# Kernel tuning notes

Measured on AMD Instinct MI355X. Metric: run time of the kernel, lower is better.

Reference implementation:

```python
import jax, jax.numpy as jnp
import numpy as np

D_MODEL = 1024
N_HEADS = 16
HEAD_DIM = D_MODEL // N_HEADS


def setup_inputs() -> dict:
    key = jax.random.key(0)
    ks = jax.random.split(key, 5)
    B, S = 2, 2048
    x = jax.random.normal(ks[0], (B, S, D_MODEL), dtype=jnp.float32)
    # nn.Linear weights: [out_features, in_features]
    s_in = 1.0 / np.sqrt(D_MODEL)
    qkv_w = jax.random.uniform(ks[1], (3 * D_MODEL, D_MODEL), jnp.float32, -s_in, s_in)
    qkv_b = jax.random.uniform(ks[2], (3 * D_MODEL,), jnp.float32, -s_in, s_in)
    out_w = jax.random.uniform(ks[3], (D_MODEL, D_MODEL), jnp.float32, -s_in, s_in)
    out_b = jax.random.uniform(ks[4], (D_MODEL,), jnp.float32, -s_in, s_in)
    return {"x": x, "qkv_w": qkv_w, "qkv_b": qkv_b, "out_w": out_w, "out_b": out_b}


def reference(x, qkv_w, qkv_b, out_w, out_b):
    B, S, D = x.shape
    H, Hd = N_HEADS, HEAD_DIM
    scale = 1.0 / np.sqrt(Hd)
    qkv = jnp.einsum('bsd,ed->bse', x, qkv_w) + qkv_b  # [B,S,3D]
    qkv = qkv.reshape(B, S, 3, H, Hd)
    q = qkv[:, :, 0].transpose(0, 2, 1, 3)  # [B,H,S,Hd]
    k = qkv[:, :, 1].transpose(0, 2, 1, 3)
    v = qkv[:, :, 2].transpose(0, 2, 1, 3)
    scores = jnp.einsum('bhqd,bhkd->bhqk', q, k) * scale  # [B,H,S,S]
    causal = jnp.triu(jnp.ones((S, S), dtype=bool), k=1)
    scores = jnp.where(causal[None, None], -jnp.inf, scores)
    probs = jax.nn.softmax(scores, axis=-1)
    out = jnp.einsum('bhqk,bhkd->bhqd', probs, v)  # [B,H,S,Hd]
    out = out.transpose(0, 2, 1, 3).reshape(B, S, D)
    out = jnp.einsum('bsd,ed->bse', out, out_w) + out_b
    return out
```

## Files before the change

### kernel.cpp

```cpp
#include <hip/hip_runtime.h>
#include <hip/hip_bf16.h>

#define SEQ    2048
#define DMODEL 1024
#define NHEAD  16
#define HDIM   64
#define BATCH  2
#define NTOK   (BATCH * SEQ)

#define N_X   (NTOK * DMODEL)
#define N_WQ  (3 * DMODEL * DMODEL)
#define N_BQ  (3 * DMODEL)
#define N_WO  (DMODEL * DMODEL)
#define N_BO  (DMODEL)
#define N_CANON (N_X + N_WQ + N_BQ + N_WO + N_BO)

#define NEG_SENT (-1.0e30f)
#define QSCALE 0.1803368801111f

typedef __attribute__((ext_vector_type(8))) short short8;
typedef __attribute__((ext_vector_type(4))) short short4v;
typedef __attribute__((ext_vector_type(4))) float f32x4;

#define MFMA_BF16(A, B, C) __builtin_amdgcn_mfma_f32_16x16x32_bf16((A), (B), (C), 0, 0, 0)

static __device__ __forceinline__ short8 load8(const __hip_bfloat16* p) {
    return *(const short8*)p;
}

static __device__ __forceinline__ void async16(const void* g, void* l) {
    __builtin_amdgcn_global_load_lds(
        (const __attribute__((address_space(1))) unsigned int*)g,
        (__attribute__((address_space(3))) unsigned int*)l,
        16, 0, 0);
}

__global__ void detect_kernel(const unsigned short* __restrict__ w, int* flag) {
    int cnt = 0;
    for (int i = threadIdx.x; i < 512; i += 64) {
        const unsigned e = (w[i] >> 7) & 0xFF;
        if (e >= 125) cnt++;
    }
#pragma unroll
    for (int o = 32; o; o >>= 1) cnt += __shfl_down(cnt, o);
    if (threadIdx.x == 0) *flag = (cnt > 8) ? 1 : 0;
}

__global__ __launch_bounds__(256) void canon_kernel(
    const void* __restrict__ s0, const void* __restrict__ s1,
    const void* __restrict__ s2, const void* __restrict__ s3,
    const void* __restrict__ s4,
    __hip_bfloat16* __restrict__ dst, const int* __restrict__ flag)
{
    const int idx = blockIdx.x * 256 + threadIdx.x;
    if (idx >= N_CANON) return;
    const void* src;
    int off;
    if (idx < N_X)                         { src = s0; off = idx; }
    else if (idx < N_X + N_WQ)             { src = s1; off = idx - N_X; }
    else if (idx < N_X + N_WQ + N_BQ)      { src = s2; off = idx - (N_X + N_WQ); }
    else if (idx < N_X + N_WQ + N_BQ + N_WO){ src = s3; off = idx - (N_X + N_WQ + N_BQ); }
    else                                   { src = s4; off = idx - (N_X + N_WQ + N_BQ + N_WO); }
    const bool isf32 = (*flag != 0);
    const float v = isf32 ? ((const float*)src)[off]
                          : __bfloat162float(((const __hip_bfloat16*)src)[off]);
    dst[idx] = __float2bfloat16(v);
}

__global__ __launch_bounds__(256) void qkv_gemm_kernel(
    const __hip_bfloat16* __restrict__ X,
    const __hip_bfloat16* __restrict__ W,
    const __hip_bfloat16* __restrict__ bias,
    __hip_bfloat16* __restrict__ Qs,
    __hip_bfloat16* __restrict__ Kb,
    __hip_bfloat16* __restrict__ Vt)
{
    constexpr int Kd = DMODEL;
    __shared__ __align__(16) __hip_bfloat16 As[128 * 32];
    __shared__ __align__(16) __hip_bfloat16 Bs[128 * 32];

    const int tid   = threadIdx.x;
    const int lane  = tid & 63;
    const int w     = tid >> 6;
    const int mTile = blockIdx.y * 128;
    const int nTile = blockIdx.x * 128;
    const int wm    = (w >> 1) * 64;
    const int wn    = (w & 1) * 64;
    const int lm    = lane & 15;
    const int lk    = (lane >> 4) * 8;

    f32x4 acc[4][4];
#pragma unroll
    for (int i = 0; i < 4; ++i)
#pragma unroll
        for (int j = 0; j < 4; ++j)
            acc[i][j] = (f32x4){0.f, 0.f, 0.f, 0.f};

    const int r0c = tid >> 2, p0c = tid & 3;
    const int r1c = (tid + 256) >> 2, p1c = tid & 3;

    for (int k0 = 0; k0 < Kd; k0 += 32) {
        __syncthreads();
        async16(&X[(size_t)(mTile + r0c) * Kd + k0 + p0c * 8], (char*)As + tid * 16);
        async16(&X[(size_t)(mTile + r1c) * Kd + k0 + p1c * 8], (char*)As + tid * 16 + 4096);
        async16(&W[(size_t)(nTile + r0c) * Kd + k0 + p0c * 8], (char*)Bs + tid * 16);
        async16(&W[(size_t)(nTile + r1c) * Kd + k0 + p1c * 8], (char*)Bs + tid * 16 + 4096);
        __syncthreads();

        short8 a[4], b[4];
#pragma unroll
        for (int i = 0; i < 4; ++i)
            a[i] = *(const short8*)&As[(wm + i * 16 + lm) * 32 + lk];
#pragma unroll
        for (int j = 0; j < 4; ++j)
            b[j] = *(const short8*)&Bs[(wn + j * 16 + lm) * 32 + lk];
#pragma unroll
        for (int i = 0; i < 4; ++i)
#pragma unroll
            for (int j = 0; j < 4; ++j)
                acc[i][j] = MFMA_BF16(a[i], b[j], acc[i][j]);
    }

    const int r0 = (lane >> 4) * 4;
#pragma unroll
    for (int j = 0; j < 4; ++j) {
        const int n  = nTile + wn + j * 16 + lm;
        const float bv = __bfloat162float(bias[n]);
        const int c = n >> 10;
        const int h = (n >> 6) & 15;
        const int d = n & 63;
#pragma unroll
        for (int i = 0; i < 4; ++i) {
#pragma unroll
            for (int r = 0; r < 4; ++r) {
                const int m  = mTile + wm + i * 16 + r0 + r;
                const int bb = m >> 11;
                const int s  = m & (SEQ - 1);
                const int bh = bb * NHEAD + h;
                const float v = acc[i][j][r] + bv;
                if (c == 0) {
                    Qs[(size_t)(bh * SEQ + s) * HDIM + d] = __float2bfloat16(v * QSCALE);
                } else if (c == 1) {
                    Kb[(size_t)(bh * SEQ + s) * HDIM + d] = __float2bfloat16(v);
                } else {
                    Vt[(size_t)(bh * HDIM + d) * SEQ + s] = __float2bfloat16(v);
                }
            }
        }
    }
}

#define P_PITCH 72
__global__ __launch_bounds__(512, 2) void attn_kernel(
    const __hip_bfloat16* __restrict__ Qs,
    const __hip_bfloat16* __restrict__ Kb,
    const __hip_bfloat16* __restrict__ Vt,
    __hip_bfloat16* __restrict__ O)
{
    __shared__ __align__(16) __hip_bfloat16 Kt[2][64 * 64];
    __shared__ __align__(16) __hip_bfloat16 Vs[2][64 * 64];
    __shared__ __align__(16) __hip_bfloat16 Pall[8][16 * P_PITCH];

    const int tid  = threadIdx.x;
    const int lane = tid & 63;
    const int wv   = tid >> 6;
    const int pr   = blockIdx.x;
    const int bh   = blockIdx.y;

    const int lm  = lane & 15;
    const int q4  = lane >> 4;
    const int lk  = q4 * 8;
    const int swz = (lm & 3) << 4;

    __hip_bfloat16* P = Pall[wv];

    const __hip_bfloat16* Qbh = Qs + (size_t)bh * SEQ * HDIM;
    const __hip_bfloat16* Kbh = Kb + (size_t)bh * SEQ * HDIM;
    const __hip_bfloat16* Vbh = Vt + (size_t)bh * HDIM * SEQ;

    const int srow = tid >> 3;
    const int scb  = (tid & 7) ^ (srow & 7);

    const int b  = bh >> 4;
    const int hh = bh & 15;

    for (int ph = 0; ph < 2; ++ph) {
        const int qb    = ph ? pr : 15 - pr;
        const int wbase = qb * 128 + wv * 16;

        short8 qa[2];
#pragma unroll
        for (int h = 0; h < 2; ++h)
            qa[h] = load8(&Qbh[(size_t)(wbase + lm) * HDIM + h * 32 + lk]);

        float m_run = NEG_SENT;
        float l_run = 0.f;
        f32x4 Oacc[4];
#pragma unroll
        for (int t = 0; t < 4; ++t) Oacc[t] = (f32x4){0.f, 0.f, 0.f, 0.f};

        const int nChunks = 2 * (qb + 1);
        int cur = 0;

        async16(&Kbh[(size_t)srow * HDIM + scb * 8], (char*)Kt[0] + tid * 16);
        async16(&Vbh[(size_t)srow * SEQ + scb * 8],  (char*)Vs[0] + tid * 16);

        for (int c = 0; c < nChunks; ++c) {
            const int k0 = c * 64;

            if (c + 1 < nChunks) {
                const int k1 = k0 + 64;
                async16(&Kbh[(size_t)(k1 + srow) * HDIM + scb * 8],
                        (char*)Kt[cur ^ 1] + tid * 16);
                async16(&Vbh[(size_t)srow * SEQ + k1 + scb * 8],
                        (char*)Vs[cur ^ 1] + tid * 16);
                asm volatile("s_waitcnt vmcnt(2)" ::: "memory");
            } else {
                asm volatile("s_waitcnt vmcnt(0)" ::: "memory");
            }
            __builtin_amdgcn_s_barrier();
            __builtin_amdgcn_sched_barrier(0);

            if (k0 <= wbase + 15) {
                const __hip_bfloat16* Kc = Kt[cur];
                const __hip_bfloat16* Vc = Vs[cur];

                short8 ka[4][2];
#pragma unroll
                for (int t = 0; t < 4; ++t)
#pragma unroll
                    for (int h = 0; h < 2; ++h)
                        ka[t][h] = *(const short8*)&Kc[(t * 16 + lm) * 64 +
                                                       (((h * 4 + q4) ^ (lm & 7)) * 8)];

                f32x4 sc[4];
#pragma unroll
                for (int t = 0; t < 4; ++t) sc[t] = (f32x4){0.f, 0.f, 0.f, 0.f};
#pragma unroll
                for (int t = 0; t < 4; ++t) {
                    sc[t] = MFMA_BF16(ka[t][0], qa[0], sc[t]);
                    sc[t] = MFMA_BF16(ka[t][1], qa[1], sc[t]);
                }

                if (k0 + 63 > wbase) {
                    const int row = wbase + lm;
#pragma unroll
                    for (int t = 0; t < 4; ++t)
#pragma unroll
                        for (int r = 0; r < 4; ++r) {
                            const int key = k0 + t * 16 + q4 * 4 + r;
                            if (key > row) sc[t][r] = NEG_SENT;
                        }
                }

                float mx = sc[0][0];
#pragma unroll
                for (int t = 0; t < 4; ++t)
#pragma unroll
                    for (int r = 0; r < 4; ++r) mx = fmaxf(mx, sc[t][r]);
                mx = fmaxf(mx, __shfl_xor(mx, 16));
                mx = fmaxf(mx, __shfl_xor(mx, 32));
                const float mn = fmaxf(m_run, mx);
                const float alpha = exp2f(m_run - mn);
                float s = 0.f;
#pragma unroll
                for (int t = 0; t < 4; ++t)
#pragma unroll
                    for (int r = 0; r < 4; ++r) {
                        const float p = exp2f(sc[t][r] - mn);
                        sc[t][r] = p;
                        s += p;
                    }
                s += __shfl_xor(s, 16);
                s += __shfl_xor(s, 32);
                l_run = l_run * alpha + s;
                m_run = mn;

#pragma unroll
                for (int r = 0; r < 4; ++r) {
                    const float av = __shfl(alpha, q4 * 4 + r);
#pragma unroll
                    for (int t = 0; t < 4; ++t) Oacc[t][r] *= av;
                }

#pragma unroll
                for (int t = 0; t < 4; ++t) {
                    short4v pk;
#pragma unroll
                    for (int r = 0; r < 4; ++r)
                        pk[r] = (short)__bfloat16_as_ushort(__float2bfloat16(sc[t][r]));
                    const int col = (t * 16 + q4 * 4) ^ swz;
                    *(short4v*)&P[lm * P_PITCH + col] = pk;
                }

#pragma unroll
                for (int h = 0; h < 2; ++h) {
                    const short8 pa = *(const short8*)&P[lm * P_PITCH + ((h * 32 + lk) ^ swz)];
#pragma unroll
                    for (int t = 0; t < 4; ++t) {
                        const short8 vb = *(const short8*)&Vc[(t * 16 + lm) * 64 +
                                                              (((h * 4 + q4) ^ (lm & 7)) * 8)];
                        Oacc[t] = MFMA_BF16(pa, vb, Oacc[t]);
                    }
                }
            }

            __builtin_amdgcn_s_barrier();
            cur ^= 1;
        }

#pragma unroll
        for (int r = 0; r < 4; ++r) {
            const float lv = __shfl(l_run, q4 * 4 + r);
            const float inv = 1.0f / lv;
            const size_t m = (size_t)b * SEQ + wbase + q4 * 4 + r;
#pragma unroll
            for (int t = 0; t < 4; ++t)
                O[m * DMODEL + hh * 64 + t * 16 + lm] = __float2bfloat16(Oacc[t][r] * inv);
        }
    }
}

__global__ __launch_bounds__(256) void proj_gemm_kernel(
    const __hip_bfloat16* __restrict__ A,
    const __hip_bfloat16* __restrict__ W,
    const __hip_bfloat16* __restrict__ bias,
    void* __restrict__ outv,
    const int* __restrict__ flag)
{
    constexpr int Kd = DMODEL;
    __shared__ __align__(16) __hip_bfloat16 As[128 * 32];
    __shared__ __align__(16) __hip_bfloat16 Bs[128 * 32];

    const int tid   = threadIdx.x;
    const int lane  = tid & 63;
    const int w     = tid >> 6;
    const int mTile = blockIdx.y * 128;
    const int nTile = blockIdx.x * 128;
    const int wm    = (w >> 1) * 64;
    const int wn    = (w & 1) * 64;
    const int lm    = lane & 15;
    const int lk    = (lane >> 4) * 8;
    const bool f32out = (*flag != 0);

    f32x4 acc[4][4];
#pragma unroll
    for (int i = 0; i < 4; ++i)
#pragma unroll
        for (int j = 0; j < 4; ++j)
            acc[i][j] = (f32x4){0.f, 0.f, 0.f, 0.f};

    const int r0c = tid >> 2, p0c = tid & 3;
    const int r1c = (tid + 256) >> 2, p1c = tid & 3;

    for (int k0 = 0; k0 < Kd; k0 += 32) {
        __syncthreads();
        async16(&A[(size_t)(mTile + r0c) * Kd + k0 + p0c * 8], (char*)As + tid * 16);
        async16(&A[(size_t)(mTile + r1c) * Kd + k0 + p1c * 8], (char*)As + tid * 16 + 4096);
        async16(&W[(size_t)(nTile + r0c) * Kd + k0 + p0c * 8], (char*)Bs + tid * 16);
        async16(&W[(size_t)(nTile + r1c) * Kd + k0 + p1c * 8], (char*)Bs + tid * 16 + 4096);
        __syncthreads();

        short8 a[4], b[4];
#pragma unroll
        for (int i = 0; i < 4; ++i)
            a[i] = *(const short8*)&As[(wm + i * 16 + lm) * 32 + lk];
#pragma unroll
        for (int j = 0; j < 4; ++j)
            b[j] = *(const short8*)&Bs[(wn + j * 16 + lm) * 32 + lk];
#pragma unroll
        for (int i = 0; i < 4; ++i)
#pragma unroll
            for (int j = 0; j < 4; ++j)
                acc[i][j] = MFMA_BF16(a[i], b[j], acc[i][j]);
    }

    const int r0 = (lane >> 4) * 4;
#pragma unroll
    for (int j = 0; j < 4; ++j) {
        const int n = nTile + wn + j * 16 + lm;
        const float bv = __bfloat162float(bias[n]);
#pragma unroll
        for (int i = 0; i < 4; ++i) {
#pragma unroll
            for (int r = 0; r < 4; ++r) {
                const size_t m = mTile + wm + i * 16 + r0 + r;
                const float v = acc[i][j][r] + bv;
                if (f32out) ((float*)outv)[m * DMODEL + n] = v;
                else ((__hip_bfloat16*)outv)[m * DMODEL + n] = __float2bfloat16(v);
            }
        }
    }
}

extern "C" void kernel_launch(void* const* d_in, const int* in_sizes, int n_in,
                              void* d_out, int out_size, void* d_ws, size_t ws_size,
                              hipStream_t stream) {
    const size_t OFF_CANON = 256;
    const size_t OFF_QS = OFF_CANON + (size_t)N_CANON * 2;
    const size_t OFF_KB = OFF_QS + (size_t)NTOK * DMODEL * 2;
    const size_t OFF_VT = OFF_KB + (size_t)NTOK * DMODEL * 2;
    const size_t OFF_AO = OFF_VT + (size_t)NTOK * DMODEL * 2;

    char* wsb = (char*)d_ws;
    int* flag = (int*)wsb;
    __hip_bfloat16* canon = (__hip_bfloat16*)(wsb + OFF_CANON);
    __hip_bfloat16* Xc = canon;
    __hip_bfloat16* Wq = Xc + N_X;
    __hip_bfloat16* Bq = Wq + N_WQ;
    __hip_bfloat16* Wo = Bq + N_BQ;
    __hip_bfloat16* Bo = Wo + N_WO;
    __hip_bfloat16* Qs = (__hip_bfloat16*)(wsb + OFF_QS);
    __hip_bfloat16* Kb = (__hip_bfloat16*)(wsb + OFF_KB);
    __hip_bfloat16* Vt = (__hip_bfloat16*)(wsb + OFF_VT);
    __hip_bfloat16* Ao = (__hip_bfloat16*)(wsb + OFF_AO);

    detect_kernel<<<1, 64, 0, stream>>>((const unsigned short*)d_in[1], flag);
    canon_kernel<<<(N_CANON + 255) / 256, 256, 0, stream>>>(
        d_in[0], d_in[1], d_in[2], d_in[3], d_in[4], canon, flag);

    {
        dim3 grid(3 * DMODEL / 128, NTOK / 128);
        qkv_gemm_kernel<<<grid, 256, 0, stream>>>(Xc, Wq, Bq, Qs, Kb, Vt);
    }
    {
        dim3 grid(8, BATCH * NHEAD);
        attn_kernel<<<grid, 512, 0, stream>>>(Qs, Kb, Vt, Ao);
    }
    {
        dim3 grid(DMODEL / 128, NTOK / 128);
        proj_gemm_kernel<<<grid, 256, 0, stream>>>(Ao, Wo, Bo, d_out, flag);
    }
}
```

Before: 218.5 us.

## Split attention keys across two workgroups and merge partials in a separate kernel

The attention grid is doubled so each query block's causal key range is split in half across two workgroups. Each writes unnormalized fp32 partial outputs plus running max and sum, and a new merge kernel combines them with log-sum-exp rescaling before writing bf16. This targets low occupancy: the old grid had only 256 workgroups of 512 threads. The change also skips the online-softmax rescale when the max grows by 8 or less (log2 domain) and raises the launch-bounds occupancy hint. The cost is an extra kernel launch and fp32 partial traffic. The lazy rescale also allows larger exponent values before normalization.

```diff
diff --git a/kernel.cpp b/kernel.cpp
--- a/kernel.cpp
+++ b/kernel.cpp
@@ -151,11 +151,12 @@
 }
 
 #define P_PITCH 72
-__global__ __launch_bounds__(512, 2) void attn_kernel(
+__global__ __launch_bounds__(512, 4) void attn_kernel(
     const __hip_bfloat16* __restrict__ Qs,
     const __hip_bfloat16* __restrict__ Kb,
     const __hip_bfloat16* __restrict__ Vt,
-    __hip_bfloat16* __restrict__ O)
+    float* __restrict__ Opart,
+    float* __restrict__ MLpart)
 {
     __shared__ __align__(16) __hip_bfloat16 Kt[2][64 * 64];
     __shared__ __align__(16) __hip_bfloat16 Vs[2][64 * 64];
@@ -164,8 +165,10 @@
     const int tid  = threadIdx.x;
     const int lane = tid & 63;
     const int wv   = tid >> 6;
-    const int pr   = blockIdx.x;
+    const int p    = blockIdx.x >> 1;
+    const int kh   = blockIdx.x & 1;
     const int bh   = blockIdx.y;
+    const int wgid = bh * 16 + blockIdx.x;
 
     const int lm  = lane & 15;
     const int q4  = lane >> 4;
@@ -181,12 +184,11 @@
     const int srow = tid >> 3;
     const int scb  = (tid & 7) ^ (srow & 7);
 
-    const int b  = bh >> 4;
-    const int hh = bh & 15;
-
     for (int ph = 0; ph < 2; ++ph) {
-        const int qb    = ph ? pr : 15 - pr;
+        const int qb    = ph ? p : 15 - p;
         const int wbase = qb * 128 + wv * 16;
+        const int nCh   = qb + 1;
+        const int c0    = kh * nCh;
 
         short8 qa[2];
 #pragma unroll
@@ -199,16 +201,15 @@
 #pragma unroll
         for (int t = 0; t < 4; ++t) Oacc[t] = (f32x4){0.f, 0.f, 0.f, 0.f};
 
-        const int nChunks = 2 * (qb + 1);
         int cur = 0;
 
-        async16(&Kbh[(size_t)srow * HDIM + scb * 8], (char*)Kt[0] + tid * 16);
-        async16(&Vbh[(size_t)srow * SEQ + scb * 8],  (char*)Vs[0] + tid * 16);
-
-        for (int c = 0; c < nChunks; ++c) {
-            const int k0 = c * 64;
-
-            if (c + 1 < nChunks) {
+        async16(&Kbh[(size_t)(c0 * 64 + srow) * HDIM + scb * 8], (char*)Kt[0] + tid * 16);
+        async16(&Vbh[(size_t)srow * SEQ + c0 * 64 + scb * 8],    (char*)Vs[0] + tid * 16);
+
+        for (int ci = 0; ci < nCh; ++ci) {
+            const int k0 = (c0 + ci) * 64;
+
+            if (ci + 1 < nCh) {
                 const int k1 = k0 + 64;
                 async16(&Kbh[(size_t)(k1 + srow) * HDIM + scb * 8],
                         (char*)Kt[cur ^ 1] + tid * 16);
@@ -260,28 +261,32 @@
                     for (int r = 0; r < 4; ++r) mx = fmaxf(mx, sc[t][r]);
                 mx = fmaxf(mx, __shfl_xor(mx, 16));
                 mx = fmaxf(mx, __shfl_xor(mx, 32));
-                const float mn = fmaxf(m_run, mx);
-                const float alpha = exp2f(m_run - mn);
+
+                if (!__all(mx <= m_run + 8.0f)) {
+                    const float mn = fmaxf(m_run, mx);
+                    const float alpha = exp2f(m_run - mn);
+                    m_run = mn;
+                    l_run *= alpha;
+#pragma unroll
+                    for (int r = 0; r < 4; ++r) {
+                        const float av = __shfl(alpha, q4 * 4 + r);
+#pragma unroll
+                        for (int t = 0; t < 4; ++t) Oacc[t][r] *= av;
+                    }
+                }
+
                 float s = 0.f;
 #pragma unroll
                 for (int t = 0; t < 4; ++t)
 #pragma unroll
                     for (int r = 0; r < 4; ++r) {
-                        const float p = exp2f(sc[t][r] - mn);
-                        sc[t][r] = p;
-                        s += p;
+                        const float pv = exp2f(sc[t][r] - m_run);
+                        sc[t][r] = pv;
+                        s += pv;
                     }
                 s += __shfl_xor(s, 16);
                 s += __shfl_xor(s, 32);
-                l_run = l_run * alpha + s;
-                m_run = mn;
-
-#pragma unroll
-                for (int r = 0; r < 4; ++r) {
-                    const float av = __shfl(alpha, q4 * 4 + r);
-#pragma unroll
-                    for (int t = 0; t < 4; ++t) Oacc[t][r] *= av;
-                }
+                l_run += s;
 
 #pragma unroll
                 for (int t = 0; t < 4; ++t) {
@@ -309,16 +314,57 @@
             cur ^= 1;
         }
 
-#pragma unroll
-        for (int r = 0; r < 4; ++r) {
-            const float lv = __shfl(l_run, q4 * 4 + r);
-            const float inv = 1.0f / lv;
-            const size_t m = (size_t)b * SEQ + wbase + q4 * 4 + r;
-#pragma unroll
-            for (int t = 0; t < 4; ++t)
-                O[m * DMODEL + hh * 64 + t * 16 + lm] = __float2bfloat16(Oacc[t][r] * inv);
+        const size_t pbase = ((size_t)wgid * 2 + ph) * 128;
+#pragma unroll
+        for (int t = 0; t < 4; ++t)
+#pragma unroll
+            for (int r = 0; r < 4; ++r)
+                Opart[(pbase + wv * 16 + q4 * 4 + r) * 64 + t * 16 + lm] = Oacc[t][r];
+        if (lane < 16) {
+            MLpart[(pbase + wv * 16 + lane) * 2 + 0] = m_run;
+            MLpart[(pbase + wv * 16 + lane) * 2 + 1] = l_run;
         }
     }
+}
+
+__global__ __launch_bounds__(256) void attn_merge_kernel(
+    const float* __restrict__ Opart, const float* __restrict__ MLpart,
+    __hip_bfloat16* __restrict__ O)
+{
+    const int idx  = blockIdx.x * 256 + threadIdx.x;
+    const int d16  = idx & 3;
+    const int grow = idx >> 2;
+    const int bh   = grow >> 11;
+    const int s    = grow & 2047;
+    const int qb   = s >> 7;
+    const int rin  = s & 127;
+    const int p    = (qb >= 8) ? (15 - qb) : qb;
+    const int ph   = (qb >= 8) ? 0 : 1;
+    const size_t r0 = ((size_t)(bh * 16 + p * 2 + 0) * 2 + ph) * 128 + rin;
+    const size_t r1 = ((size_t)(bh * 16 + p * 2 + 1) * 2 + ph) * 128 + rin;
+
+    const float m1 = MLpart[r0 * 2], l1 = MLpart[r0 * 2 + 1];
+    const float m2 = MLpart[r1 * 2], l2 = MLpart[r1 * 2 + 1];
+    const float mm = fmaxf(m1, m2);
+    const float a1 = exp2f(m1 - mm), a2 = exp2f(m2 - mm);
+    const float inv = 1.0f / (a1 * l1 + a2 * l2);
+
+    const f32x4* O1 = (const f32x4*)&Opart[r0 * 64 + d16 * 16];
+    const f32x4* O2 = (const f32x4*)&Opart[r1 * 64 + d16 * 16];
+
+    short8 out[2];
+#pragma unroll
+    for (int v = 0; v < 4; ++v) {
+        const f32x4 x1 = O1[v], x2 = O2[v];
+#pragma unroll
+        for (int j = 0; j < 4; ++j)
+            out[v >> 1][(v & 1) * 4 + j] = (short)__bfloat16_as_ushort(
+                __float2bfloat16((a1 * x1[j] + a2 * x2[j]) * inv));
+    }
+    const int b = bh >> 4, hh = bh & 15;
+    __hip_bfloat16* dst = &O[((size_t)b * SEQ + s) * DMODEL + hh * 64 + d16 * 16];
+    ((short8*)dst)[0] = out[0];
+    ((short8*)dst)[1] = out[1];
 }
 
 __global__ __launch_bounds__(256) void proj_gemm_kernel(
@@ -401,6 +447,8 @@
     const size_t OFF_KB = OFF_QS + (size_t)NTOK * DMODEL * 2;
     const size_t OFF_VT = OFF_KB + (size_t)NTOK * DMODEL * 2;
     const size_t OFF_AO = OFF_VT + (size_t)NTOK * DMODEL * 2;
+    const size_t OFF_OP = OFF_AO + (size_t)NTOK * DMODEL * 2;
+    const size_t OFF_ML = OFF_OP + (size_t)512 * 2 * 128 * 64 * 4;
 
     char* wsb = (char*)d_ws;
     int* flag = (int*)wsb;
@@ -414,6 +462,8 @@
     __hip_bfloat16* Kb = (__hip_bfloat16*)(wsb + OFF_KB);
     __hip_bfloat16* Vt = (__hip_bfloat16*)(wsb + OFF_VT);
     __hip_bfloat16* Ao = (__hip_bfloat16*)(wsb + OFF_AO);
+    float* Opart = (float*)(wsb + OFF_OP);
+    float* MLpart = (float*)(wsb + OFF_ML);
 
     detect_kernel<<<1, 64, 0, stream>>>((const unsigned short*)d_in[1], flag);
     canon_kernel<<<(N_CANON + 255) / 256, 256, 0, stream>>>(
@@ -424,8 +474,10 @@
         qkv_gemm_kernel<<<grid, 256, 0, stream>>>(Xc, Wq, Bq, Qs, Kb, Vt);
     }
     {
-        dim3 grid(8, BATCH * NHEAD);
-        attn_kernel<<<grid, 512, 0, stream>>>(Qs, Kb, Vt, Ao);
+        dim3 grid(16, BATCH * NHEAD);
+        attn_kernel<<<grid, 512, 0, stream>>>(Qs, Kb, Vt, Opart, MLpart);
+        attn_merge_kernel<<<(NTOK * NHEAD * 4) / 256, 256, 0, stream>>>(
+            Opart, MLpart, Ao);
     }
     {
         dim3 grid(DMODEL / 128, NTOK / 128);
```

Result: faster. 212.9 us (-2.6%).
